# Performance work log

Hardware: AMD Instinct MI355X
Metric: run time of the kernel (lower is better)

The kernel has to match this reference:

```python
import jax, jax.numpy as jnp
import numpy as np

B = 16          # graphs per batch
NN = 2000       # nodes per graph (num_nodes)
N = B * NN      # total nodes in the batched graph
F_IN = 128      # input node features
H, C = 4, 64    # heads, per-head out channels (both GAT layers)
HC = H * C
DEG = 12        # average degree per node
FC1, FC2, OUT = 512, 128, 1
FC_IN = 6 * NN  # len(which_layer) = 6


def setup_inputs() -> dict:
    key = jax.random.key(0)
    ks = jax.random.split(key, 32)

    def g(i, shape, s=0.05):
        return jax.random.normal(ks[i], shape, jnp.float32) * s

    # within-graph random edges, no self loops (GATConv removes then re-adds them)
    src_l = jax.random.randint(ks[0], (B, NN * DEG), 0, NN)
    off = jax.random.randint(ks[1], (B, NN * DEG), 1, NN)
    dst_l = (src_l + off) % NN
    goff = (jnp.arange(B) * NN)[:, None]
    edge_index = jnp.stack([(src_l + goff).reshape(-1),
                            (dst_l + goff).reshape(-1)]).astype(jnp.int32)

    return {
        "x": g(2, (N, F_IN), 1.0),
        "W1": g(3, (F_IN, HC)), "att_src1": g(4, (H, C)), "att_dst1": g(5, (H, C)),
        "b1": jnp.zeros((HC,), jnp.float32),
        "W2": g(6, (HC, HC)), "att_src2": g(7, (H, C)), "att_dst2": g(8, (H, C)),
        "b2": jnp.zeros((HC,), jnp.float32),
        "pw1": g(9, (HC, 1)), "pb1": jnp.zeros((1,), jnp.float32),
        "pw2": g(10, (HC, 1)), "pb2": jnp.zeros((1,), jnp.float32),
        "ln_w": jnp.ones((NN,), jnp.float32), "ln_b": jnp.zeros((NN,), jnp.float32),
        "sex_emb": g(11, (2, NN)), "mut_emb": g(12, (4, NN)),
        "age_w": g(13, (NN,)), "age_b": jnp.zeros((NN,), jnp.float32),
        "fw1": g(14, (FC_IN, FC1)), "fb1": jnp.zeros((FC1,), jnp.float32),
        "fw2": g(15, (FC1, FC2)), "fb2": jnp.zeros((FC2,), jnp.float32),
        "fw3": g(16, (FC2, OUT)), "fb3": jnp.zeros((OUT,), jnp.float32),
        "age": jax.random.uniform(ks[17], (B,), jnp.float32),
        "edge_index": edge_index,
        "sex": jax.random.randint(ks[18], (B,), 0, 2),
        "mutation": jax.random.randint(ks[19], (B,), 0, 4),
    }


def _layer_norm(x, w, b, eps=1e-5):
    mu = jnp.mean(x, -1, keepdims=True)
    var = jnp.mean((x - mu) ** 2, -1, keepdims=True)
    return (x - mu) / jnp.sqrt(var + eps) * w + b


def _gat_conv(x, W, att_src, att_dst, bias, src, dst):
    h = (x @ W).reshape(N, H, C)                         # [N,H,C]
    a_s = jnp.sum(h * att_src[None], -1)                 # [N,H]
    a_d = jnp.sum(h * att_dst[None], -1)                 # [N,H]
    alpha = jax.nn.leaky_relu(a_s[src] + a_d[dst], 0.2)  # [E,H]
    m = jax.ops.segment_max(alpha, dst, num_segments=N)  # segment softmax over dst
    e = jnp.exp(alpha - m[dst])
    denom = jax.ops.segment_sum(e, dst, num_segments=N)
    a = e / (denom[dst] + 1e-16)
    out = jax.ops.segment_sum(a[:, :, None] * h[src], dst, num_segments=N)
    return out.reshape(N, HC) + bias


def _forward(x, W1, att_src1, att_dst1, b1, W2, att_src2, att_dst2, b2,
             pw1, pb1, pw2, pb2, ln_w, ln_b, sex_emb, mut_emb, age_w, age_b,
             fw1, fb1, fw2, fb2, fw3, fb3, age, edge_index, sex, mutation):
    loop = jnp.arange(N, dtype=edge_index.dtype)         # self loops added by GATConv
    src = jnp.concatenate([edge_index[0], loop])
    dst = jnp.concatenate([edge_index[1], loop])

    x0 = jnp.mean(x, -1).reshape(B, NN)                  # to_dense_batch(mean(x,-1))

    h = jax.nn.relu(_gat_conv(x, W1, att_src1, att_dst1, b1, src, dst))
    x1 = (h @ pw1 + pb1).squeeze(-1).reshape(B, NN)
    h = jax.nn.relu(_gat_conv(h, W2, att_src2, att_dst2, b2, src, dst))
    x2 = (h @ pw2 + pb2).squeeze(-1).reshape(B, NN)

    x0 = _layer_norm(x0, ln_w, ln_b)
    x1 = _layer_norm(x1, ln_w, ln_b)
    x2 = _layer_norm(x2, ln_w, ln_b)
    ms = jnp.concatenate([x0, x1, x2], axis=1)           # [B, 3*NN]

    demo = jnp.concatenate([sex_emb[sex], mut_emb[mutation],
                            age[:, None] * age_w[None, :] + age_b], axis=1)
    t = jnp.concatenate([demo, ms], axis=1)              # [B, 6*NN]
    t = jax.nn.relu(t @ fw1 + fb1)
    t = jax.nn.relu(t @ fw2 + fb2)
    pred = t @ fw3 + fb3                                 # [B, 1]
    return pred, x0, x1, x2, ms


def reference(x, W1, att_src1, att_dst1, b1, W2, att_src2, att_dst2, b2,
              pw1, pb1, pw2, pb2, ln_w, ln_b, sex_emb, mut_emb, age_w, age_b,
              fw1, fb1, fw2, fb2, fw3, fb3, age, edge_index, sex, mutation):
    return _forward(x, W1, att_src1, att_dst1, b1, W2, att_src2, att_dst2, b2,
                    pw1, pb1, pw2, pb2, ln_w, ln_b, sex_emb, mut_emb, age_w, age_b,
                    fw1, fb1, fw2, fb2, fw3, fb3, age, edge_index, sex, mutation)
```

## Files before the change

kernel.cpp:

```cpp
#include <hip/hip_runtime.h>
#include <math.h>

#define NTOT   32000
#define NNODE  2000
#define NB     16
#define FIN    128
#define HCDIM  256
#define NH     4
#define FC1DIM 512
#define FC2DIM 128
#define FCIN   12000
#define KC1    50
#define NCH1   240
#define CAP    64
#define BK     32
#define LPITCH 40

typedef __attribute__((ext_vector_type(8))) short bf16x8;
typedef __attribute__((ext_vector_type(4))) float f32x4;

__device__ inline float4 ld4(const float* p){ return *reinterpret_cast<const float4*>(p); }
__device__ inline void st4(float* p, float4 v){ *reinterpret_cast<float4*>(p) = v; }
__device__ inline float4 add4(float4 a, float4 b){ return make_float4(a.x+b.x,a.y+b.y,a.z+b.z,a.w+b.w); }
__device__ inline float4 max4(float4 a, float4 b){ return make_float4(fmaxf(a.x,b.x),fmaxf(a.y,b.y),fmaxf(a.z,b.z),fmaxf(a.w,b.w)); }
__device__ inline float lrelu(float x){ return x > 0.f ? x : 0.2f*x; }
__device__ inline float4 leaky4(float4 a){ return make_float4(lrelu(a.x),lrelu(a.y),lrelu(a.z),lrelu(a.w)); }
__device__ inline float4 exp4s(float4 a, float4 m){ return make_float4(__expf(a.x-m.x),__expf(a.y-m.y),__expf(a.z-m.z),__expf(a.w-m.w)); }
__device__ inline float dot4(float4 a, float4 b){ return a.x*b.x + a.y*b.y + a.z*b.z + a.w*b.w; }
__device__ inline float selh(float4 v, int h){ return h==0 ? v.x : (h==1 ? v.y : (h==2 ? v.z : v.w)); }

__device__ inline unsigned short f2bf(float f){
  unsigned int u = __float_as_uint(f);
  u += 0x7FFFu + ((u >> 16) & 1u);
  return (unsigned short)(u >> 16);
}
__device__ inline float bf2f(unsigned short h){
  return __uint_as_float(((unsigned int)h) << 16);
}
__device__ inline float4 ldbf4(const unsigned short* p){
  ushort4 v = *reinterpret_cast<const ushort4*>(p);
  return make_float4(bf2f(v.x), bf2f(v.y), bf2f(v.z), bf2f(v.w));
}

__device__ inline float4 redmax4_64(float4 m){
  #pragma unroll
  for(int off=1; off<64; off<<=1){
    m.x = fmaxf(m.x, __shfl_xor(m.x, off));
    m.y = fmaxf(m.y, __shfl_xor(m.y, off));
    m.z = fmaxf(m.z, __shfl_xor(m.z, off));
    m.w = fmaxf(m.w, __shfl_xor(m.w, off));
  }
  return m;
}
__device__ inline float4 redsum4_64(float4 d){
  #pragma unroll
  for(int off=1; off<64; off<<=1){
    d.x += __shfl_xor(d.x, off);
    d.y += __shfl_xor(d.y, off);
    d.z += __shfl_xor(d.z, off);
    d.w += __shfl_xor(d.w, off);
  }
  return d;
}

__global__ __launch_bounds__(256) void k_prep(const float* __restrict__ x,
                                              unsigned short* __restrict__ xb,
                                              float* __restrict__ x0r,
                                              int* __restrict__ cnt){
  int gid = blockIdx.x*256 + threadIdx.x;
  if(gid < NTOT) cnt[gid] = 0;
  int lane = threadIdx.x & 63, wv = threadIdx.x >> 6;
  int n = blockIdx.x*4 + wv;
  const float* r = x + (size_t)n*FIN;
  float2 v = *reinterpret_cast<const float2*>(r + lane*2);
  unsigned int packed = (unsigned int)f2bf(v.x) | ((unsigned int)f2bf(v.y) << 16);
  *reinterpret_cast<unsigned int*>(xb + (size_t)n*FIN + lane*2) = packed;
  float s = v.x + v.y;
  #pragma unroll
  for(int off=1; off<64; off<<=1) s += __shfl_xor(s, off);
  if(lane == 0) x0r[n] = s * (1.0f/FIN);
}

__global__ void k_build(const int* __restrict__ src, const int* __restrict__ dst,
                        int* __restrict__ cnt, int* __restrict__ col, int e0){
  int i = blockIdx.x*blockDim.x + threadIdx.x;
  if(i < e0){
    int d = dst[i];
    int slot = atomicAdd(&cnt[d], 1);
    if(slot < CAP) col[(d<<6) + slot] = src[i];
  }
}

__global__ void k_tr2(const float* __restrict__ W1, const float* __restrict__ W2,
                      unsigned short* __restrict__ W1t, unsigned short* __restrict__ W2t){
  int idx = blockIdx.x*blockDim.x + threadIdx.x;
  if(idx < HCDIM*FIN){
    int n = idx / FIN, k = idx - n*FIN;
    W1t[idx] = f2bf(W1[(size_t)k*HCDIM + n]);
  } else {
    int j = idx - HCDIM*FIN;
    int n = j / HCDIM, k = j - n*HCDIM;
    W2t[j] = f2bf(W2[(size_t)k*HCDIM + n]);
  }
}

__global__ __launch_bounds__(256) void k_gemm_bf(const unsigned short* __restrict__ A,
                                                 const unsigned short* __restrict__ Bt,
                                                 unsigned short* __restrict__ C,
                                                 const float* __restrict__ attS,
                                                 const float* __restrict__ attD,
                                                 float* __restrict__ a_s,
                                                 float* __restrict__ a_d,
                                                 int M, int K){
  __shared__ unsigned short As[128][LPITCH];
  __shared__ unsigned short Bs[128][LPITCH];
  int tid = threadIdx.x;
  int lane = tid & 63, wv = tid >> 6;
  int wm = (wv & 1)*64, wn = (wv >> 1)*64;
  int m0 = blockIdx.y*128, n0 = blockIdx.x*128;
  int l15 = lane & 15, lq = lane >> 4;
  f32x4 acc[4][4];
  #pragma unroll
  for(int i=0;i<4;i++)
    #pragma unroll
    for(int j=0;j<4;j++)
      acc[i][j] = (f32x4){0.f,0.f,0.f,0.f};

  int r = tid >> 2, c = (tid & 3)*8;
  for(int k0 = 0; k0 < K; k0 += BK){
    *reinterpret_cast<uint4*>(&As[r][c])    = *reinterpret_cast<const uint4*>(A  + (size_t)(m0+r)*K + k0 + c);
    *reinterpret_cast<uint4*>(&As[r+64][c]) = *reinterpret_cast<const uint4*>(A  + (size_t)(m0+r+64)*K + k0 + c);
    *reinterpret_cast<uint4*>(&Bs[r][c])    = *reinterpret_cast<const uint4*>(Bt + (size_t)(n0+r)*K + k0 + c);
    *reinterpret_cast<uint4*>(&Bs[r+64][c]) = *reinterpret_cast<const uint4*>(Bt + (size_t)(n0+r+64)*K + k0 + c);
    __syncthreads();
    bf16x8 af[4], bfr[4];
    #pragma unroll
    for(int i=0;i<4;i++){
      af[i]  = *reinterpret_cast<const bf16x8*>(&As[wm + i*16 + l15][lq*8]);
      bfr[i] = *reinterpret_cast<const bf16x8*>(&Bs[wn + i*16 + l15][lq*8]);
    }
    #pragma unroll
    for(int mi=0;mi<4;mi++)
      #pragma unroll
      for(int ni=0;ni<4;ni++)
        acc[mi][ni] = __builtin_amdgcn_mfma_f32_16x16x32_bf16(af[mi], bfr[ni], acc[mi][ni], 0, 0, 0);
    __syncthreads();
  }
  #pragma unroll
  for(int mi=0;mi<4;mi++){
    #pragma unroll
    for(int ni=0;ni<4;ni++){
      int cn = n0 + wn + ni*16 + l15;
      #pragma unroll
      for(int rg=0;rg<4;rg++){
        int rm = m0 + wm + mi*16 + lq*4 + rg;
        C[(size_t)rm*HCDIM + cn] = f2bf(acc[mi][ni][rg]);
      }
    }
  }
  int head = (n0 + wn) >> 6;
  float avs[4], avd[4];
  #pragma unroll
  for(int ni=0;ni<4;ni++){
    int cc = ni*16 + l15;
    avs[ni] = attS[head*64 + cc];
    avd[ni] = attD[head*64 + cc];
  }
  #pragma unroll
  for(int mi=0;mi<4;mi++){
    #pragma unroll
    for(int rg=0;rg<4;rg++){
      float ps = 0.f, pd = 0.f;
      #pragma unroll
      for(int ni=0;ni<4;ni++){
        float v = acc[mi][ni][rg];
        ps = fmaf(avs[ni], v, ps);
        pd = fmaf(avd[ni], v, pd);
      }
      #pragma unroll
      for(int off=1; off<16; off<<=1){
        ps += __shfl_xor(ps, off);
        pd += __shfl_xor(pd, off);
      }
      if(l15 == 0){
        int rm = m0 + wm + mi*16 + lq*4 + rg;
        a_s[rm*4 + head] = ps;
        a_d[rm*4 + head] = pd;
      }
    }
  }
}

template<int STORE>
__global__ __launch_bounds__(256) void k_agg(const unsigned short* __restrict__ hpre,
                                             const float* __restrict__ a_s,
                                             const float* __restrict__ a_d,
                                             const int* __restrict__ cnt,
                                             const int* __restrict__ col,
                                             const float* __restrict__ bias,
                                             const float* __restrict__ pw,
                                             const float* __restrict__ pb,
                                             unsigned short* __restrict__ hout,
                                             float* __restrict__ xraw){
  __shared__ float4 ew[4][CAP];
  int tid = threadIdx.x;
  int lane = tid & 63, wv = tid >> 6;
  int blk  = blockIdx.x;
  int xcd  = blk & 7;
  int slot = blk >> 3;
  int half = slot / 500;
  int g    = xcd + 8*half;
  int n    = g*NNODE + (slot - half*500)*4 + wv;
  int f0 = lane*4;
  int hl = lane >> 4;
  float4 ad   = ld4(a_d + n*4);
  float4 asn  = ld4(a_s + n*4);
  float4 aself = leaky4(add4(asn, ad));
  float4 m = aself;
  int deg = min(cnt[n], CAP);
  int base = n << 6;
  if(lane < deg){
    int s = col[base + lane];
    m = max4(m, leaky4(add4(ld4(a_s + s*4), ad)));
  }
  m = redmax4_64(m);
  float4 d;
  if(lane < deg){
    int s = col[base + lane];
    float4 al = leaky4(add4(ld4(a_s + s*4), ad));
    float4 ex = exp4s(al, m);
    ew[wv][lane] = ex;
    d = ex;
  } else {
    d = make_float4(0.f,0.f,0.f,0.f);
  }
  if(lane == 0) d = add4(d, exp4s(aself, m));
  d = redsum4_64(d);
  float invh = 1.0f / (selh(d, hl) + 1e-16f);
  float wself = __expf(selh(aself, hl) - selh(m, hl)) * invh;
  float4 hv = ldbf4(hpre + (size_t)n*HCDIM + f0);
  float4 acc = make_float4(wself*hv.x, wself*hv.y, wself*hv.z, wself*hv.w);
  __syncthreads();
  const float* ewf = (const float*)&ew[wv][0];
  for(int e = 0; e < deg; e++){
    int s = col[base + e];
    float w = ewf[e*4 + hl] * invh;
    float4 h2 = ldbf4(hpre + (size_t)s*HCDIM + f0);
    acc.x = fmaf(w, h2.x, acc.x); acc.y = fmaf(w, h2.y, acc.y);
    acc.z = fmaf(w, h2.z, acc.z); acc.w = fmaf(w, h2.w, acc.w);
  }
  float4 b4 = ld4(bias + f0);
  acc = make_float4(fmaxf(acc.x+b4.x,0.f), fmaxf(acc.y+b4.y,0.f),
                    fmaxf(acc.z+b4.z,0.f), fmaxf(acc.w+b4.w,0.f));
  if(STORE){
    ushort4 hb = make_ushort4(f2bf(acc.x), f2bf(acc.y), f2bf(acc.z), f2bf(acc.w));
    *reinterpret_cast<ushort4*>(hout + (size_t)n*HCDIM + f0) = hb;
  }
  float part = dot4(acc, ld4(pw + f0));
  #pragma unroll
  for(int off=1; off<64; off<<=1) part += __shfl_xor(part, off);
  if(lane == 0) xraw[n] = part + pb[0];
}

__global__ __launch_bounds__(256) void k_ln3(const float* __restrict__ xraw0,
                                             const float* __restrict__ lnw,
                                             const float* __restrict__ lnb,
                                             float* __restrict__ out,
                                             float* __restrict__ t){
  int blk = blockIdx.x;
  int b = blk & 15, which = blk >> 4;
  const float* src = xraw0 + which*NTOT + b*NNODE;
  __shared__ float red[8];
  int tid = threadIdx.x, lane = tid & 63, wv = tid >> 6;
  float s = 0.f, ss = 0.f;
  for(int i = tid; i < NNODE; i += 256){ float v = src[i]; s += v; ss += v*v; }
  #pragma unroll
  for(int off=1; off<64; off<<=1){ s += __shfl_xor(s, off); ss += __shfl_xor(ss, off); }
  if(lane == 0){ red[wv] = s; red[4+wv] = ss; }
  __syncthreads();
  s  = red[0]+red[1]+red[2]+red[3];
  ss = red[4]+red[5]+red[6]+red[7];
  float mu  = s * (1.0f/NNODE);
  float var = ss * (1.0f/NNODE) - mu*mu;
  float inv = 1.0f / sqrtf(var + 1e-5f);
  float* o1 = out + 16 + which*(NB*NNODE) + b*NNODE;
  float* o2 = out + 16 + 3*(NB*NNODE) + b*(3*NNODE) + which*NNODE;
  float* o3 = t + b*FCIN + 3*NNODE + which*NNODE;
  for(int i = tid; i < NNODE; i += 256){
    float v = (src[i]-mu)*inv*lnw[i] + lnb[i];
    o1[i] = v; o2[i] = v; o3[i] = v;
  }
}

__global__ void k_demo(const float* __restrict__ sexemb, const float* __restrict__ mutemb,
                       const float* __restrict__ agew, const float* __restrict__ ageb,
                       const float* __restrict__ age, const int* __restrict__ sex,
                       const int* __restrict__ mut, float* __restrict__ t){
  int i = blockIdx.x*blockDim.x + threadIdx.x;
  int b = i / (3*NNODE);
  int j = i - b*(3*NNODE);
  float v;
  if(j < NNODE)          v = sexemb[sex[b]*NNODE + j];
  else if(j < 2*NNODE)   v = mutemb[mut[b]*NNODE + (j - NNODE)];
  else                   v = age[b]*agew[j - 2*NNODE] + ageb[j - 2*NNODE];
  t[b*FCIN + j] = v;
}

__global__ __launch_bounds__(256) void k_fc1p(const float* __restrict__ t,
                                              const float* __restrict__ fw1,
                                              float* __restrict__ partial){
  __shared__ float ts[NB][KC1];
  __shared__ float red[NB][FC1DIM];
  int tid = threadIdx.x;
  int half = tid >> 7;
  int c4 = (tid & 127) * 4;
  int k0 = blockIdx.x * KC1;
  for(int i = tid; i < NB*KC1; i += 256){
    int b = i / KC1, kk = i - b*KC1;
    ts[b][kk] = t[b*FCIN + k0 + kk];
  }
  __syncthreads();
  float4 acc[NB];
  #pragma unroll
  for(int b=0;b<NB;b++) acc[b] = make_float4(0.f,0.f,0.f,0.f);
  for(int kk = half; kk < KC1; kk += 2){
    float4 w = ld4(fw1 + (size_t)(k0+kk)*FC1DIM + c4);
    #pragma unroll
    for(int b=0;b<NB;b++){
      float tv = ts[b][kk];
      acc[b].x = fmaf(tv, w.x, acc[b].x);
      acc[b].y = fmaf(tv, w.y, acc[b].y);
      acc[b].z = fmaf(tv, w.z, acc[b].z);
      acc[b].w = fmaf(tv, w.w, acc[b].w);
    }
  }
  if(half == 1){
    #pragma unroll
    for(int b=0;b<NB;b++) st4(&red[b][c4], acc[b]);
  }
  __syncthreads();
  if(half == 0){
    float* po = partial + (size_t)blockIdx.x*(NB*FC1DIM);
    #pragma unroll
    for(int b=0;b<NB;b++){
      float4 r = ld4(&red[b][c4]);
      st4(po + b*FC1DIM + c4, add4(acc[b], r));
    }
  }
}

__global__ void k_fc1r(const float* __restrict__ partial, const float* __restrict__ fb1,
                       float* __restrict__ t1){
  int i = blockIdx.x*blockDim.x + threadIdx.x;
  float s = fb1[i & (FC1DIM-1)];
  for(int c=0;c<NCH1;c++) s += partial[(size_t)c*(NB*FC1DIM) + i];
  t1[i] = fmaxf(s, 0.f);
}

__global__ __launch_bounds__(128) void k_head2(const float* __restrict__ t1,
                                               const float* __restrict__ fw2,
                                               const float* __restrict__ fb2,
                                               const float* __restrict__ fw3,
                                               const float* __restrict__ fb3,
                                               float* __restrict__ pred){
  __shared__ float red[2];
  int b = blockIdx.x, j = threadIdx.x;
  const float* tr = t1 + b*FC1DIM;
  float s = fb2[j];
  for(int k=0;k<FC1DIM;k++) s = fmaf(tr[k], fw2[k*FC2DIM+j], s);
  s = fmaxf(s, 0.f) * fw3[j];
  #pragma unroll
  for(int off=1; off<64; off<<=1) s += __shfl_xor(s, off);
  int lane = j & 63, wv = j >> 6;
  if(lane == 0) red[wv] = s;
  __syncthreads();
  if(j == 0) pred[b] = red[0] + red[1] + fb3[0];
}

extern "C" void kernel_launch(void* const* d_in, const int* in_sizes, int n_in,
                              void* d_out, int out_size, void* d_ws, size_t ws_size,
                              hipStream_t stream) {
  const float* x       = (const float*)d_in[0];
  const float* W1      = (const float*)d_in[1];
  const float* attS1   = (const float*)d_in[2];
  const float* attD1   = (const float*)d_in[3];
  const float* b1      = (const float*)d_in[4];
  const float* W2      = (const float*)d_in[5];
  const float* attS2   = (const float*)d_in[6];
  const float* attD2   = (const float*)d_in[7];
  const float* b2      = (const float*)d_in[8];
  const float* pw1     = (const float*)d_in[9];
  const float* pb1     = (const float*)d_in[10];
  const float* pw2     = (const float*)d_in[11];
  const float* pb2     = (const float*)d_in[12];
  const float* lnw     = (const float*)d_in[13];
  const float* lnb     = (const float*)d_in[14];
  const float* sexemb  = (const float*)d_in[15];
  const float* mutemb  = (const float*)d_in[16];
  const float* agew    = (const float*)d_in[17];
  const float* ageb    = (const float*)d_in[18];
  const float* fw1     = (const float*)d_in[19];
  const float* fb1     = (const float*)d_in[20];
  const float* fw2     = (const float*)d_in[21];
  const float* fb2     = (const float*)d_in[22];
  const float* fw3     = (const float*)d_in[23];
  const float* fb3     = (const float*)d_in[24];
  const float* age     = (const float*)d_in[25];
  const int*   eidx    = (const int*)d_in[26];
  const int*   sex     = (const int*)d_in[27];
  const int*   mut     = (const int*)d_in[28];
  const int E0 = in_sizes[26] / 2;
  const int* esrc = eidx;
  const int* edst = eidx + E0;

  float* out = (float*)d_out;

  float* w = (float*)d_ws;
  float* a_s  = w;
  float* a_d  = a_s + NTOT*NH;
  float* x0r  = a_d + NTOT*NH;
  float* x1r  = x0r + NTOT;
  float* x2r  = x1r + NTOT;
  float* tbuf = x2r + NTOT;
  float* part = tbuf + NB*FCIN;
  float* t1   = part + (size_t)NCH1*NB*FC1DIM;
  unsigned short* xb  = (unsigned short*)(t1 + NB*FC1DIM);
  unsigned short* hA  = xb  + (size_t)NTOT*FIN;
  unsigned short* hB  = hA  + (size_t)NTOT*HCDIM;
  unsigned short* W1t = hB  + (size_t)NTOT*HCDIM;
  unsigned short* W2t = W1t + HCDIM*FIN;
  int* cnt    = (int*)(W2t + HCDIM*HCDIM);
  int* col    = cnt + NTOT;
  (void)ws_size; (void)n_in; (void)out_size;

  const int eb = (E0 + 255)/256;

  k_prep<<<NTOT/4, 256, 0, stream>>>(x, xb, x0r, cnt);
  k_build<<<eb, 256, 0, stream>>>(esrc, edst, cnt, col, E0);
  k_tr2<<<(HCDIM*FIN + HCDIM*HCDIM)/256, 256, 0, stream>>>(W1, W2, W1t, W2t);

  k_gemm_bf<<<dim3(HCDIM/128, NTOT/128), 256, 0, stream>>>(xb, W1t, hA, attS1, attD1, a_s, a_d, NTOT, FIN);
  k_agg<1><<<NTOT/4, 256, 0, stream>>>(hA, a_s, a_d, cnt, col, b1, pw1, pb1, hB, x1r);

  k_gemm_bf<<<dim3(HCDIM/128, NTOT/128), 256, 0, stream>>>(hB, W2t, hA, attS2, attD2, a_s, a_d, NTOT, HCDIM);
  k_agg<0><<<NTOT/4, 256, 0, stream>>>(hA, a_s, a_d, cnt, col, b2, pw2, pb2, hB, x2r);

  k_demo<<<(NB*3*NNODE)/256, 256, 0, stream>>>(sexemb, mutemb, agew, ageb, age, sex, mut, tbuf);
  k_ln3<<<3*NB, 256, 0, stream>>>(x0r, lnw, lnb, out, tbuf);

  k_fc1p<<<NCH1, 256, 0, stream>>>(tbuf, fw1, part);
  k_fc1r<<<(NB*FC1DIM)/256, 256, 0, stream>>>(part, fb1, t1);
  k_head2<<<NB, 128, 0, stream>>>(t1, fw2, fb2, fw3, fb3, out);
}
```

Before: 292.1 us.

## Merge setup kernels, drop softmax max pass, atomically reduce FC1 partials

Four small setup kernels (edge CSR build, weight transpose, demographic fill, and a new zeroing of t1) are merged into one launch. The GAT aggregation no longer subtracts the max before exponentiating, so the max and sum shuffle reductions disappear. Column indices are staged in shared memory, the barrier is removed, and normalisation is applied once at the end. FC1 partial sums are accumulated into t1 with atomics instead of a separate reduction kernel, and bias plus ReLU move into k_head2. The costs are possible exp overflow without max subtraction, non-deterministic float atomic ordering, and contention on the FC1 atomics.

```diff
diff --git a/kernel.cpp b/kernel.cpp
--- a/kernel.cpp
+++ b/kernel.cpp
@@ -15,6 +15,9 @@
 #define CAP    64
 #define BK     32
 #define LPITCH 40
+#define TRB    384
+#define DEMOB  375
+#define T1B    32
 
 typedef __attribute__((ext_vector_type(8))) short bf16x8;
 typedef __attribute__((ext_vector_type(4))) float f32x4;
@@ -22,10 +25,9 @@
 __device__ inline float4 ld4(const float* p){ return *reinterpret_cast<const float4*>(p); }
 __device__ inline void st4(float* p, float4 v){ *reinterpret_cast<float4*>(p) = v; }
 __device__ inline float4 add4(float4 a, float4 b){ return make_float4(a.x+b.x,a.y+b.y,a.z+b.z,a.w+b.w); }
-__device__ inline float4 max4(float4 a, float4 b){ return make_float4(fmaxf(a.x,b.x),fmaxf(a.y,b.y),fmaxf(a.z,b.z),fmaxf(a.w,b.w)); }
 __device__ inline float lrelu(float x){ return x > 0.f ? x : 0.2f*x; }
 __device__ inline float4 leaky4(float4 a){ return make_float4(lrelu(a.x),lrelu(a.y),lrelu(a.z),lrelu(a.w)); }
-__device__ inline float4 exp4s(float4 a, float4 m){ return make_float4(__expf(a.x-m.x),__expf(a.y-m.y),__expf(a.z-m.z),__expf(a.w-m.w)); }
+__device__ inline float4 exp4u(float4 a){ return make_float4(__expf(a.x),__expf(a.y),__expf(a.z),__expf(a.w)); }
 __device__ inline float dot4(float4 a, float4 b){ return a.x*b.x + a.y*b.y + a.z*b.z + a.w*b.w; }
 __device__ inline float selh(float4 v, int h){ return h==0 ? v.x : (h==1 ? v.y : (h==2 ? v.z : v.w)); }
 
@@ -40,27 +42,6 @@
 __device__ inline float4 ldbf4(const unsigned short* p){
   ushort4 v = *reinterpret_cast<const ushort4*>(p);
   return make_float4(bf2f(v.x), bf2f(v.y), bf2f(v.z), bf2f(v.w));
-}
-
-__device__ inline float4 redmax4_64(float4 m){
-  #pragma unroll
-  for(int off=1; off<64; off<<=1){
-    m.x = fmaxf(m.x, __shfl_xor(m.x, off));
-    m.y = fmaxf(m.y, __shfl_xor(m.y, off));
-    m.z = fmaxf(m.z, __shfl_xor(m.z, off));
-    m.w = fmaxf(m.w, __shfl_xor(m.w, off));
-  }
-  return m;
-}
-__device__ inline float4 redsum4_64(float4 d){
-  #pragma unroll
-  for(int off=1; off<64; off<<=1){
-    d.x += __shfl_xor(d.x, off);
-    d.y += __shfl_xor(d.y, off);
-    d.z += __shfl_xor(d.z, off);
-    d.w += __shfl_xor(d.w, off);
-  }
-  return d;
 }
 
 __global__ __launch_bounds__(256) void k_prep(const float* __restrict__ x,
@@ -81,26 +62,45 @@
   if(lane == 0) x0r[n] = s * (1.0f/FIN);
 }
 
-__global__ void k_build(const int* __restrict__ src, const int* __restrict__ dst,
-                        int* __restrict__ cnt, int* __restrict__ col, int e0){
-  int i = blockIdx.x*blockDim.x + threadIdx.x;
-  if(i < e0){
-    int d = dst[i];
-    int slot = atomicAdd(&cnt[d], 1);
-    if(slot < CAP) col[(d<<6) + slot] = src[i];
-  }
-}
-
-__global__ void k_tr2(const float* __restrict__ W1, const float* __restrict__ W2,
-                      unsigned short* __restrict__ W1t, unsigned short* __restrict__ W2t){
-  int idx = blockIdx.x*blockDim.x + threadIdx.x;
-  if(idx < HCDIM*FIN){
-    int n = idx / FIN, k = idx - n*FIN;
-    W1t[idx] = f2bf(W1[(size_t)k*HCDIM + n]);
+__global__ void k_misc(const int* __restrict__ src, const int* __restrict__ dst,
+                       int* __restrict__ cnt, int* __restrict__ col, int e0, int eb,
+                       const float* __restrict__ W1, const float* __restrict__ W2,
+                       unsigned short* __restrict__ W1t, unsigned short* __restrict__ W2t,
+                       const float* __restrict__ sexemb, const float* __restrict__ mutemb,
+                       const float* __restrict__ agew, const float* __restrict__ ageb,
+                       const float* __restrict__ age, const int* __restrict__ sex,
+                       const int* __restrict__ mut, float* __restrict__ t,
+                       float* __restrict__ t1){
+  int blk = blockIdx.x;
+  if(blk < eb){
+    int i = blk*256 + threadIdx.x;
+    if(i < e0){
+      int d = dst[i];
+      int slot = atomicAdd(&cnt[d], 1);
+      if(slot < CAP) col[(d<<6) + slot] = src[i];
+    }
+  } else if(blk < eb + TRB){
+    int idx = (blk - eb)*256 + threadIdx.x;
+    if(idx < HCDIM*FIN){
+      int n = idx / FIN, k = idx - n*FIN;
+      W1t[idx] = f2bf(W1[(size_t)k*HCDIM + n]);
+    } else {
+      int j = idx - HCDIM*FIN;
+      int n = j / HCDIM, k = j - n*HCDIM;
+      W2t[j] = f2bf(W2[(size_t)k*HCDIM + n]);
+    }
+  } else if(blk < eb + TRB + DEMOB){
+    int i = (blk - eb - TRB)*256 + threadIdx.x;
+    int b = i / (3*NNODE);
+    int j = i - b*(3*NNODE);
+    float v;
+    if(j < NNODE)          v = sexemb[sex[b]*NNODE + j];
+    else if(j < 2*NNODE)   v = mutemb[mut[b]*NNODE + (j - NNODE)];
+    else                   v = age[b]*agew[j - 2*NNODE] + ageb[j - 2*NNODE];
+    t[b*FCIN + j] = v;
   } else {
-    int j = idx - HCDIM*FIN;
-    int n = j / HCDIM, k = j - n*HCDIM;
-    W2t[j] = f2bf(W2[(size_t)k*HCDIM + n]);
+    int i = (blk - eb - TRB - DEMOB)*256 + threadIdx.x;
+    t1[i] = 0.f;
   }
 }
 
@@ -203,6 +203,7 @@
                                              unsigned short* __restrict__ hout,
                                              float* __restrict__ xraw){
   __shared__ float4 ew[4][CAP];
+  __shared__ int    cols[4][CAP];
   int tid = threadIdx.x;
   int lane = tid & 63, wv = tid >> 6;
   int blk  = blockIdx.x;
@@ -215,43 +216,32 @@
   int hl = lane >> 4;
   float4 ad   = ld4(a_d + n*4);
   float4 asn  = ld4(a_s + n*4);
-  float4 aself = leaky4(add4(asn, ad));
-  float4 m = aself;
+  float4 eself = exp4u(leaky4(add4(asn, ad)));
   int deg = min(cnt[n], CAP);
   int base = n << 6;
   if(lane < deg){
     int s = col[base + lane];
-    m = max4(m, leaky4(add4(ld4(a_s + s*4), ad)));
-  }
-  m = redmax4_64(m);
-  float4 d;
-  if(lane < deg){
-    int s = col[base + lane];
-    float4 al = leaky4(add4(ld4(a_s + s*4), ad));
-    float4 ex = exp4s(al, m);
-    ew[wv][lane] = ex;
-    d = ex;
-  } else {
-    d = make_float4(0.f,0.f,0.f,0.f);
-  }
-  if(lane == 0) d = add4(d, exp4s(aself, m));
-  d = redsum4_64(d);
-  float invh = 1.0f / (selh(d, hl) + 1e-16f);
-  float wself = __expf(selh(aself, hl) - selh(m, hl)) * invh;
+    cols[wv][lane] = s;
+    ew[wv][lane] = exp4u(leaky4(add4(ld4(a_s + s*4), ad)));
+  }
+  float es = selh(eself, hl);
+  float dsum = es;
   float4 hv = ldbf4(hpre + (size_t)n*HCDIM + f0);
-  float4 acc = make_float4(wself*hv.x, wself*hv.y, wself*hv.z, wself*hv.w);
-  __syncthreads();
+  float4 acc = make_float4(es*hv.x, es*hv.y, es*hv.z, es*hv.w);
   const float* ewf = (const float*)&ew[wv][0];
+  const int*   cwf = &cols[wv][0];
   for(int e = 0; e < deg; e++){
-    int s = col[base + e];
-    float w = ewf[e*4 + hl] * invh;
+    int s = cwf[e];
+    float w = ewf[e*4 + hl];
+    dsum += w;
     float4 h2 = ldbf4(hpre + (size_t)s*HCDIM + f0);
     acc.x = fmaf(w, h2.x, acc.x); acc.y = fmaf(w, h2.y, acc.y);
     acc.z = fmaf(w, h2.z, acc.z); acc.w = fmaf(w, h2.w, acc.w);
   }
+  float invh = 1.0f / (dsum + 1e-16f);
   float4 b4 = ld4(bias + f0);
-  acc = make_float4(fmaxf(acc.x+b4.x,0.f), fmaxf(acc.y+b4.y,0.f),
-                    fmaxf(acc.z+b4.z,0.f), fmaxf(acc.w+b4.w,0.f));
+  acc = make_float4(fmaxf(fmaf(acc.x,invh,b4.x),0.f), fmaxf(fmaf(acc.y,invh,b4.y),0.f),
+                    fmaxf(fmaf(acc.z,invh,b4.z),0.f), fmaxf(fmaf(acc.w,invh,b4.w),0.f));
   if(STORE){
     ushort4 hb = make_ushort4(f2bf(acc.x), f2bf(acc.y), f2bf(acc.z), f2bf(acc.w));
     *reinterpret_cast<ushort4*>(hout + (size_t)n*HCDIM + f0) = hb;
@@ -292,23 +282,9 @@
   }
 }
 
-__global__ void k_demo(const float* __restrict__ sexemb, const float* __restrict__ mutemb,
-                       const float* __restrict__ agew, const float* __restrict__ ageb,
-                       const float* __restrict__ age, const int* __restrict__ sex,
-                       const int* __restrict__ mut, float* __restrict__ t){
-  int i = blockIdx.x*blockDim.x + threadIdx.x;
-  int b = i / (3*NNODE);
-  int j = i - b*(3*NNODE);
-  float v;
-  if(j < NNODE)          v = sexemb[sex[b]*NNODE + j];
-  else if(j < 2*NNODE)   v = mutemb[mut[b]*NNODE + (j - NNODE)];
-  else                   v = age[b]*agew[j - 2*NNODE] + ageb[j - 2*NNODE];
-  t[b*FCIN + j] = v;
-}
-
 __global__ __launch_bounds__(256) void k_fc1p(const float* __restrict__ t,
                                               const float* __restrict__ fw1,
-                                              float* __restrict__ partial){
+                                              float* __restrict__ t1){
   __shared__ float ts[NB][KC1];
   __shared__ float red[NB][FC1DIM];
   int tid = threadIdx.x;
@@ -340,32 +316,31 @@
   }
   __syncthreads();
   if(half == 0){
-    float* po = partial + (size_t)blockIdx.x*(NB*FC1DIM);
     #pragma unroll
     for(int b=0;b<NB;b++){
       float4 r = ld4(&red[b][c4]);
-      st4(po + b*FC1DIM + c4, add4(acc[b], r));
-    }
-  }
-}
-
-__global__ void k_fc1r(const float* __restrict__ partial, const float* __restrict__ fb1,
-                       float* __restrict__ t1){
-  int i = blockIdx.x*blockDim.x + threadIdx.x;
-  float s = fb1[i & (FC1DIM-1)];
-  for(int c=0;c<NCH1;c++) s += partial[(size_t)c*(NB*FC1DIM) + i];
-  t1[i] = fmaxf(s, 0.f);
+      float* dst = t1 + b*FC1DIM + c4;
+      atomicAdd(dst+0, acc[b].x + r.x);
+      atomicAdd(dst+1, acc[b].y + r.y);
+      atomicAdd(dst+2, acc[b].z + r.z);
+      atomicAdd(dst+3, acc[b].w + r.w);
+    }
+  }
 }
 
 __global__ __launch_bounds__(128) void k_head2(const float* __restrict__ t1,
+                                               const float* __restrict__ fb1,
                                                const float* __restrict__ fw2,
                                                const float* __restrict__ fb2,
                                                const float* __restrict__ fw3,
                                                const float* __restrict__ fb3,
                                                float* __restrict__ pred){
+  __shared__ float tr[FC1DIM];
   __shared__ float red[2];
   int b = blockIdx.x, j = threadIdx.x;
-  const float* tr = t1 + b*FC1DIM;
+  for(int k = j; k < FC1DIM; k += 128)
+    tr[k] = fmaxf(t1[b*FC1DIM + k] + fb1[k], 0.f);
+  __syncthreads();
   float s = fb2[j];
   for(int k=0;k<FC1DIM;k++) s = fmaf(tr[k], fw2[k*FC2DIM+j], s);
   s = fmaxf(s, 0.f) * fw3[j];
@@ -422,8 +397,7 @@
   float* x1r  = x0r + NTOT;
   float* x2r  = x1r + NTOT;
   float* tbuf = x2r + NTOT;
-  float* part = tbuf + NB*FCIN;
-  float* t1   = part + (size_t)NCH1*NB*FC1DIM;
+  float* t1   = tbuf + NB*FCIN;
   unsigned short* xb  = (unsigned short*)(t1 + NB*FC1DIM);
   unsigned short* hA  = xb  + (size_t)NTOT*FIN;
   unsigned short* hB  = hA  + (size_t)NTOT*HCDIM;
@@ -436,8 +410,10 @@
   const int eb = (E0 + 255)/256;
 
   k_prep<<<NTOT/4, 256, 0, stream>>>(x, xb, x0r, cnt);
-  k_build<<<eb, 256, 0, stream>>>(esrc, edst, cnt, col, E0);
-  k_tr2<<<(HCDIM*FIN + HCDIM*HCDIM)/256, 256, 0, stream>>>(W1, W2, W1t, W2t);
+  k_misc<<<eb + TRB + DEMOB + T1B, 256, 0, stream>>>(esrc, edst, cnt, col, E0, eb,
+                                                     W1, W2, W1t, W2t,
+                                                     sexemb, mutemb, agew, ageb,
+                                                     age, sex, mut, tbuf, t1);
 
   k_gemm_bf<<<dim3(HCDIM/128, NTOT/128), 256, 0, stream>>>(xb, W1t, hA, attS1, attD1, a_s, a_d, NTOT, FIN);
   k_agg<1><<<NTOT/4, 256, 0, stream>>>(hA, a_s, a_d, cnt, col, b1, pw1, pb1, hB, x1r);
@@ -445,10 +421,8 @@
   k_gemm_bf<<<dim3(HCDIM/128, NTOT/128), 256, 0, stream>>>(hB, W2t, hA, attS2, attD2, a_s, a_d, NTOT, HCDIM);
   k_agg<0><<<NTOT/4, 256, 0, stream>>>(hA, a_s, a_d, cnt, col, b2, pw2, pb2, hB, x2r);
 
-  k_demo<<<(NB*3*NNODE)/256, 256, 0, stream>>>(sexemb, mutemb, agew, ageb, age, sex, mut, tbuf);
   k_ln3<<<3*NB, 256, 0, stream>>>(x0r, lnw, lnb, out, tbuf);
 
-  k_fc1p<<<NCH1, 256, 0, stream>>>(tbuf, fw1, part);
-  k_fc1r<<<(NB*FC1DIM)/256, 256, 0, stream>>>(part, fb1, t1);
-  k_head2<<<NB, 128, 0, stream>>>(t1, fw2, fb2, fw3, fb3, out);
-}
+  k_fc1p<<<NCH1, 256, 0, stream>>>(tbuf, fw1, t1);
+  k_head2<<<NB, 128, 0, stream>>>(t1, fb1, fw2, fb2, fw3, fb3, out);
+}
```

After: 314.0 us. +7.5%, slower.
